# Optimization experiments

Measured on AMD Instinct MI355X. Metric: run time of the kernel, lower is better.

The kernel has to match this reference:

```python
import jax, jax.numpy as jnp
import numpy as np

N_INP = 128
N_HID = 512
N_OUT = 256
N_HEADS = 64
N_SM = 4
EPS_GN = 1e-5
TINY = 1e-14


def setup_inputs() -> dict:
    key = jax.random.key(0)
    ks = jax.random.split(key, 8)
    s = 0.05  # small init scale keeps softplus/softmax in a sane range
    f32 = jnp.float32
    return {
        "x": jax.random.normal(ks[0], (N_INP, N_INP), f32),
        "last_out_sm": jax.random.uniform(ks[1], (N_OUT, N_HEADS), f32),
        # grouped-conv weights, stored per-head with conv singleton dims squeezed
        "qw": jax.random.normal(ks[2], (N_HEADS, N_INP), f32) * s,            # Conv2d q
        "w1": jax.random.normal(ks[3], (N_HEADS, N_HID, N_INP), f32) * s,     # Conv1d l1
        "gn1_g": jnp.ones((N_HEADS, N_HID), f32),                             # GroupNorm ln_l1
        "gn1_b": jnp.zeros((N_HEADS, N_HID), f32),
        "w2": jax.random.normal(ks[4], (N_SM, N_HEADS, N_OUT, N_HID), f32) * s,  # Conv1d l2_n
        "gn2_g": jnp.ones((N_SM, N_HEADS, N_OUT), f32),                       # GroupNorm ln_l2_n
        "gn2_b": jnp.zeros((N_SM, N_HEADS, N_OUT), f32),
        "ws": jax.random.normal(ks[5], (N_HEADS, N_OUT, N_OUT), f32) * s,     # Conv1d scalar
        "woo": jax.random.normal(ks[6], (N_HEADS, 2 * N_OUT), f32) * s,       # Conv1d on_off
    }


def _group_norm(z, g, b):
    # normalize over the last (per-head channel) axis, biased variance, then affine
    mu = z.mean(-1, keepdims=True)
    var = z.var(-1, keepdims=True)
    return (z - mu) * jax.lax.rsqrt(var + EPS_GN) * g + b


def reference(x, last_out_sm, qw, w1, gn1_g, gn1_b, w2, gn2_g, gn2_b, ws, woo):
    n_out = last_out_sm.shape[0]
    # q: grouped Conv2d with kernel (1, n_inp) on replicated x -> per-head x @ qw_h
    sub = jnp.einsum("rc,hc->hr", x, qw)                     # (H, n_inp)
    # l1 (grouped 1x1 conv == per-head matmul) + GroupNorm(n_heads groups) + softplus
    h1 = jax.nn.softplus(_group_norm(jnp.einsum("hoi,hi->ho", w1, sub), gn1_g, gn1_b))  # (H, n_hid)
    # l2_n branches: per-head matmul + GroupNorm + softmax over n_out, summed over n_sm
    z = _group_norm(jnp.einsum("shoi,hi->sho", w2, h1), gn2_g, gn2_b)  # (S, H, n_out)
    out_sm = jax.nn.softmax(z, axis=-1).sum(0).T             # (n_out, H)
    # scalar branch: grouped 1x1 conv applied to ones -> row-sum of per-head weight
    scalar = ws.sum(-1).T                                    # (n_out, H)
    # on_off gate: per-head dot of [prod(last_out_sm, dim1), out_sm[:, h]] with woo_h
    last_prod = jnp.prod(last_out_sm, axis=1)                # (n_out,)
    gate_logit = woo[:, :n_out] @ last_prod + jnp.einsum("ho,oh->h", woo[:, n_out:], out_sm)
    on_off = jax.nn.sigmoid(gate_logit)                      # (H,)
    on_off_out_sm = on_off[None, :] * out_sm                 # (n_out, H)
    out_scaled = on_off_out_sm * scalar
    out_scaled = jnp.where(jnp.abs(out_scaled) <= TINY, TINY, out_scaled)
    return (jnp.clip(on_off_out_sm, TINY, None), out_scaled)
```

## Files before the change

### kernel.cpp

```cpp
#include <hip/hip_runtime.h>
#include <math.h>

#define N_INP 128
#define N_HID 512
#define N_OUT 256
#define N_HEADS 64
#define N_SM 4
#define EPS_GN 1e-5f
#define TINY 1e-14f

__device__ __forceinline__ float wave_sum(float v) {
#pragma unroll
  for (int off = 32; off; off >>= 1) v += __shfl_down(v, off);
  return v;
}
__device__ __forceinline__ float wave_max(float v) {
#pragma unroll
  for (int off = 32; off; off >>= 1) v = fmaxf(v, __shfl_down(v, off));
  return v;
}

__device__ __forceinline__ float block_sum(float v, float* red) {
  int wave = threadIdx.x >> 6, lane = threadIdx.x & 63;
  int nw = blockDim.x >> 6;
  v = wave_sum(v);
  __syncthreads();
  if (lane == 0) red[wave] = v;
  __syncthreads();
  float s = 0.f;
  for (int i = 0; i < nw; ++i) s += red[i];
  return s;
}
__device__ __forceinline__ float block_max(float v, float* red) {
  int wave = threadIdx.x >> 6, lane = threadIdx.x & 63;
  int nw = blockDim.x >> 6;
  v = wave_max(v);
  __syncthreads();
  if (lane == 0) red[wave] = v;
  __syncthreads();
  float s = -3.4e38f;
  for (int i = 0; i < nw; ++i) s = fmaxf(s, red[i]);
  return s;
}

__global__ __launch_bounds__(512) void k_head1(
    const float* __restrict__ x, const float* __restrict__ qw,
    const float* __restrict__ w1, const float* __restrict__ g1,
    const float* __restrict__ b1, float* __restrict__ h1,
    float* __restrict__ osm) {
  int h = blockIdx.x;
  int tid = threadIdx.x, wave = tid >> 6, lane = tid & 63;
  __shared__ float sub_s[N_INP];
  __shared__ float z_s[N_HID];
  __shared__ float red[8];

  if (tid < 256) osm[h * 256 + tid] = 0.f;

  float2 qv = ((const float2*)(qw + h * N_INP))[lane];
  for (int r = wave; r < N_INP; r += 8) {
    float2 xv = ((const float2*)(x + r * N_INP))[lane];
    float p = wave_sum(xv.x * qv.x + xv.y * qv.y);
    if (lane == 0) sub_s[r] = p;
  }
  __syncthreads();

  float2 sv = ((const float2*)sub_s)[lane];
  const float* w1h = w1 + (size_t)h * N_HID * N_INP;
  for (int k = 0; k < 64; ++k) {
    int o = wave * 64 + k;
    float2 wv = ((const float2*)(w1h + (size_t)o * N_INP))[lane];
    float p = wave_sum(wv.x * sv.x + wv.y * sv.y);
    if (lane == 0) z_s[o] = p;
  }
  __syncthreads();

  float v = z_s[tid];
  float s = block_sum(v, red);
  float ss = block_sum(v * v, red);
  float mu = s * (1.f / N_HID);
  float var = ss * (1.f / N_HID) - mu * mu;
  float r = rsqrtf(var + EPS_GN);
  float zz = (v - mu) * r * g1[h * N_HID + tid] + b1[h * N_HID + tid];
  h1[h * N_HID + tid] = fmaxf(zz, 0.f) + log1pf(expf(-fabsf(zz)));
}

__global__ __launch_bounds__(1024) void k_l2_scalar(
    const float* __restrict__ w2, const float* __restrict__ h1,
    const float* __restrict__ g2, const float* __restrict__ b2,
    const float* __restrict__ wsc, float* __restrict__ osm,
    float* __restrict__ scal) {
  int blk = blockIdx.x;
  int tid = threadIdx.x, wave = tid >> 6, lane = tid & 63;

  if (blk < 256) {
    int h = blk & 63;
    __shared__ float z_s[N_OUT];
    __shared__ float red[16];

    const float4* h1v = (const float4*)(h1 + h * N_HID);
    float4 ha = h1v[lane];
    float4 hb = h1v[64 + lane];
    const float* w2base = w2 + (size_t)blk * N_OUT * N_HID;
    for (int k = 0; k < 16; ++k) {
      int o = wave * 16 + k;
      const float4* row = (const float4*)(w2base + (size_t)o * N_HID);
      float4 wa = row[lane];
      float4 wb = row[64 + lane];
      float p = wa.x * ha.x + wa.y * ha.y + wa.z * ha.z + wa.w * ha.w +
                wb.x * hb.x + wb.y * hb.y + wb.z * hb.z + wb.w * hb.w;
      p = wave_sum(p);
      if (lane == 0) z_s[o] = p;
    }
    __syncthreads();

    float v = (tid < N_OUT) ? z_s[tid] : 0.f;
    float s = block_sum(v, red);
    float ss = block_sum(v * v, red);
    float mu = s * (1.f / N_OUT);
    float var = ss * (1.f / N_OUT) - mu * mu;
    float rs = rsqrtf(var + EPS_GN);
    float zn = (tid < N_OUT)
                   ? (v - mu) * rs * g2[(size_t)blk * N_OUT + tid] + b2[(size_t)blk * N_OUT + tid]
                   : -3.4e38f;
    float mx = block_max(zn, red);
    float e = (tid < N_OUT) ? expf(zn - mx) : 0.f;
    float es = block_sum(e, red);
    if (tid < N_OUT) atomicAdd(&osm[tid * N_HEADS + h], e / es);
  } else {
    int h = blk - 256;
    for (int k = 0; k < 16; ++k) {
      int o = wave * 16 + k;
      float4 v = ((const float4*)(wsc + ((size_t)(h * N_OUT + o)) * N_OUT))[lane];
      float p = wave_sum(v.x + v.y + v.z + v.w);
      if (lane == 0) scal[o * N_HEADS + h] = p;
    }
  }
}

__global__ __launch_bounds__(256) void k_gate_final(
    const float* __restrict__ last, const float* __restrict__ woo,
    const float* __restrict__ osm, const float* __restrict__ scal,
    float* __restrict__ out) {
  int h = blockIdx.x;
  int tid = threadIdx.x;
  __shared__ float red[4];

  const float4* row = (const float4*)(last + (size_t)tid * N_HEADS);
  float p = 1.f;
#pragma unroll
  for (int j = 0; j < 16; ++j) {
    float4 v = row[j];
    p *= v.x * v.y * v.z * v.w;
  }
  float o_sm = osm[tid * N_HEADS + h];
  float part = woo[h * 2 * N_OUT + tid] * p +
               woo[h * 2 * N_OUT + N_OUT + tid] * o_sm;
  float logit = block_sum(part, red);
  float oo = 1.f / (1.f + expf(-logit));

  float v0 = oo * o_sm;
  out[tid * N_HEADS + h] = fmaxf(v0, TINY);
  float v1 = v0 * scal[tid * N_HEADS + h];
  out[N_OUT * N_HEADS + tid * N_HEADS + h] = (fabsf(v1) <= TINY) ? TINY : v1;
}

extern "C" void kernel_launch(void* const* d_in, const int* in_sizes, int n_in,
                              void* d_out, int out_size, void* d_ws, size_t ws_size,
                              hipStream_t stream) {
  const float* x    = (const float*)d_in[0];
  const float* last = (const float*)d_in[1];
  const float* qw   = (const float*)d_in[2];
  const float* w1   = (const float*)d_in[3];
  const float* g1   = (const float*)d_in[4];
  const float* b1   = (const float*)d_in[5];
  const float* w2   = (const float*)d_in[6];
  const float* g2   = (const float*)d_in[7];
  const float* b2   = (const float*)d_in[8];
  const float* wsc  = (const float*)d_in[9];
  const float* woo  = (const float*)d_in[10];
  float* out = (float*)d_out;
  float* ws  = (float*)d_ws;

  float* h1   = ws;
  float* osm  = ws + 32768;
  float* scal = ws + 49152;

  hipLaunchKernelGGL(k_head1,     dim3(64),  dim3(512),  0, stream, x, qw, w1, g1, b1, h1, osm);
  hipLaunchKernelGGL(k_l2_scalar, dim3(320), dim3(1024), 0, stream, w2, h1, g2, b2, wsc, osm, scal);
  hipLaunchKernelGGL(k_gate_final,dim3(64),  dim3(256),  0, stream, last, woo, osm, scal, out);
}
```

Measured before the change: 294.7 us.

## Split l1 matmul across four blocks per head and move GroupNorm1 into l2 kernel

The first kernel now runs 256 blocks (four output quarters per head) instead of 64. Each block writes raw l1 pre-activations, so the per-head GroupNorm and softplus can no longer finish there. That normalization moves into the l2 kernel, which every (sm, head) block recomputes redundantly. The scalar row-sum work is spread over the 256 l2 blocks instead of 64 extra blocks. The aim is to fill more CUs while streaming w1, at the cost of recomputing GroupNorm1 four times per head.

```diff
diff --git a/kernel.cpp b/kernel.cpp
--- a/kernel.cpp
+++ b/kernel.cpp
@@ -43,18 +43,16 @@
   return s;
 }
 
-__global__ __launch_bounds__(512) void k_head1(
+__global__ __launch_bounds__(512) void k_z1(
     const float* __restrict__ x, const float* __restrict__ qw,
-    const float* __restrict__ w1, const float* __restrict__ g1,
-    const float* __restrict__ b1, float* __restrict__ h1,
+    const float* __restrict__ w1, float* __restrict__ z1,
     float* __restrict__ osm) {
-  int h = blockIdx.x;
+  int blk = blockIdx.x;
+  int h = blk >> 2, oq = blk & 3;
   int tid = threadIdx.x, wave = tid >> 6, lane = tid & 63;
   __shared__ float sub_s[N_INP];
-  __shared__ float z_s[N_HID];
-  __shared__ float red[8];
 
-  if (tid < 256) osm[h * 256 + tid] = 0.f;
+  if (tid < 64) osm[blk * 64 + tid] = 0.f;
 
   float2 qv = ((const float2*)(qw + h * N_INP))[lane];
   for (int r = wave; r < N_INP; r += 8) {
@@ -65,76 +63,76 @@
   __syncthreads();
 
   float2 sv = ((const float2*)sub_s)[lane];
-  const float* w1h = w1 + (size_t)h * N_HID * N_INP;
-  for (int k = 0; k < 64; ++k) {
-    int o = wave * 64 + k;
+  const float* w1h = w1 + ((size_t)h * N_HID + (size_t)oq * 128) * N_INP;
+  for (int k = 0; k < 16; ++k) {
+    int o = wave * 16 + k;
     float2 wv = ((const float2*)(w1h + (size_t)o * N_INP))[lane];
     float p = wave_sum(wv.x * sv.x + wv.y * sv.y);
+    if (lane == 0) z1[h * N_HID + oq * 128 + o] = p;
+  }
+}
+
+__global__ __launch_bounds__(1024) void k_l2_scalar(
+    const float* __restrict__ z1, const float* __restrict__ g1,
+    const float* __restrict__ b1, const float* __restrict__ w2,
+    const float* __restrict__ g2, const float* __restrict__ b2,
+    const float* __restrict__ wsc, float* __restrict__ osm,
+    float* __restrict__ scal) {
+  int blk = blockIdx.x;
+  int s = blk >> 6, h = blk & 63;
+  int tid = threadIdx.x, wave = tid >> 6, lane = tid & 63;
+  __shared__ float h1_s[N_HID];
+  __shared__ float z_s[N_OUT];
+  __shared__ float red[16];
+
+  float v1 = (tid < N_HID) ? z1[h * N_HID + tid] : 0.f;
+  float s1 = block_sum(v1, red);
+  float ss1 = block_sum(v1 * v1, red);
+  float mu1 = s1 * (1.f / N_HID);
+  float var1 = ss1 * (1.f / N_HID) - mu1 * mu1;
+  float r1 = rsqrtf(var1 + EPS_GN);
+  if (tid < N_HID) {
+    float zz = (v1 - mu1) * r1 * g1[h * N_HID + tid] + b1[h * N_HID + tid];
+    h1_s[tid] = fmaxf(zz, 0.f) + log1pf(expf(-fabsf(zz)));
+  }
+  __syncthreads();
+
+  float4 ha = ((const float4*)h1_s)[lane];
+  float4 hb = ((const float4*)h1_s)[64 + lane];
+
+  for (int k = 0; k < 4; ++k) {
+    int o = s * 64 + wave * 4 + k;
+    float4 v = ((const float4*)(wsc + ((size_t)(h * N_OUT + o)) * N_OUT))[lane];
+    float p = wave_sum(v.x + v.y + v.z + v.w);
+    if (lane == 0) scal[o * N_HEADS + h] = p;
+  }
+
+  const float* w2base = w2 + (size_t)blk * N_OUT * N_HID;
+  for (int k = 0; k < 16; ++k) {
+    int o = wave * 16 + k;
+    const float4* row = (const float4*)(w2base + (size_t)o * N_HID);
+    float4 wa = row[lane];
+    float4 wb = row[64 + lane];
+    float p = wa.x * ha.x + wa.y * ha.y + wa.z * ha.z + wa.w * ha.w +
+              wb.x * hb.x + wb.y * hb.y + wb.z * hb.z + wb.w * hb.w;
+    p = wave_sum(p);
     if (lane == 0) z_s[o] = p;
   }
   __syncthreads();
 
-  float v = z_s[tid];
-  float s = block_sum(v, red);
-  float ss = block_sum(v * v, red);
-  float mu = s * (1.f / N_HID);
-  float var = ss * (1.f / N_HID) - mu * mu;
-  float r = rsqrtf(var + EPS_GN);
-  float zz = (v - mu) * r * g1[h * N_HID + tid] + b1[h * N_HID + tid];
-  h1[h * N_HID + tid] = fmaxf(zz, 0.f) + log1pf(expf(-fabsf(zz)));
-}
-
-__global__ __launch_bounds__(1024) void k_l2_scalar(
-    const float* __restrict__ w2, const float* __restrict__ h1,
-    const float* __restrict__ g2, const float* __restrict__ b2,
-    const float* __restrict__ wsc, float* __restrict__ osm,
-    float* __restrict__ scal) {
-  int blk = blockIdx.x;
-  int tid = threadIdx.x, wave = tid >> 6, lane = tid & 63;
-
-  if (blk < 256) {
-    int h = blk & 63;
-    __shared__ float z_s[N_OUT];
-    __shared__ float red[16];
-
-    const float4* h1v = (const float4*)(h1 + h * N_HID);
-    float4 ha = h1v[lane];
-    float4 hb = h1v[64 + lane];
-    const float* w2base = w2 + (size_t)blk * N_OUT * N_HID;
-    for (int k = 0; k < 16; ++k) {
-      int o = wave * 16 + k;
-      const float4* row = (const float4*)(w2base + (size_t)o * N_HID);
-      float4 wa = row[lane];
-      float4 wb = row[64 + lane];
-      float p = wa.x * ha.x + wa.y * ha.y + wa.z * ha.z + wa.w * ha.w +
-                wb.x * hb.x + wb.y * hb.y + wb.z * hb.z + wb.w * hb.w;
-      p = wave_sum(p);
-      if (lane == 0) z_s[o] = p;
-    }
-    __syncthreads();
-
-    float v = (tid < N_OUT) ? z_s[tid] : 0.f;
-    float s = block_sum(v, red);
-    float ss = block_sum(v * v, red);
-    float mu = s * (1.f / N_OUT);
-    float var = ss * (1.f / N_OUT) - mu * mu;
-    float rs = rsqrtf(var + EPS_GN);
-    float zn = (tid < N_OUT)
-                   ? (v - mu) * rs * g2[(size_t)blk * N_OUT + tid] + b2[(size_t)blk * N_OUT + tid]
-                   : -3.4e38f;
-    float mx = block_max(zn, red);
-    float e = (tid < N_OUT) ? expf(zn - mx) : 0.f;
-    float es = block_sum(e, red);
-    if (tid < N_OUT) atomicAdd(&osm[tid * N_HEADS + h], e / es);
-  } else {
-    int h = blk - 256;
-    for (int k = 0; k < 16; ++k) {
-      int o = wave * 16 + k;
-      float4 v = ((const float4*)(wsc + ((size_t)(h * N_OUT + o)) * N_OUT))[lane];
-      float p = wave_sum(v.x + v.y + v.z + v.w);
-      if (lane == 0) scal[o * N_HEADS + h] = p;
-    }
-  }
+  float v = (tid < N_OUT) ? z_s[tid] : 0.f;
+  float sz = block_sum(v, red);
+  float ssz = block_sum(v * v, red);
+  float mu = sz * (1.f / N_OUT);
+  float var = ssz * (1.f / N_OUT) - mu * mu;
+  float rs = rsqrtf(var + EPS_GN);
+  float zn = (tid < N_OUT)
+                 ? (v - mu) * rs * g2[(size_t)blk * N_OUT + tid] + b2[(size_t)blk * N_OUT + tid]
+                 : -3.4e38f;
+  float mx = block_max(zn, red);
+  float e = (tid < N_OUT) ? expf(zn - mx) : 0.f;
+  float es = block_sum(e, red);
+  if (tid < N_OUT) atomicAdd(&osm[tid * N_HEADS + h], e / es);
 }
 
 __global__ __launch_bounds__(256) void k_gate_final(
@@ -181,11 +179,11 @@
   float* out = (float*)d_out;
   float* ws  = (float*)d_ws;
 
-  float* h1   = ws;
+  float* z1   = ws;
   float* osm  = ws + 32768;
   float* scal = ws + 49152;
 
-  hipLaunchKernelGGL(k_head1,     dim3(64),  dim3(512),  0, stream, x, qw, w1, g1, b1, h1, osm);
-  hipLaunchKernelGGL(k_l2_scalar, dim3(320), dim3(1024), 0, stream, w2, h1, g2, b2, wsc, osm, scal);
+  hipLaunchKernelGGL(k_z1,        dim3(256), dim3(512),  0, stream, x, qw, w1, z1, osm);
+  hipLaunchKernelGGL(k_l2_scalar, dim3(256), dim3(1024), 0, stream, z1, g1, b1, w2, g2, b2, wsc, osm, scal);
   hipLaunchKernelGGL(k_gate_final,dim3(64),  dim3(256),  0, stream, last, woo, osm, scal, out);
 }
```

New measurement: 262.5 us. 10.9% less time.
